# Performance work log

Hardware: AMD Instinct MI355X
Metric: run time of the kernel (lower is better)

## Reference

```python
import jax, jax.numpy as jnp
import numpy as np

N = 200000       # nodes
E = 6400000      # edges
F_IN, H1, H2, C = 7, 32, 16, 2


def gcn_conv(x, W, b, src, dst, n):
    """PyG GCNConv: add self-loops, symmetric normalization, linear, scatter-add."""
    loop = jnp.arange(n, dtype=src.dtype)
    s = jnp.concatenate([src, loop])
    d = jnp.concatenate([dst, loop])
    # degree of target nodes (with self-loops)
    deg = jax.ops.segment_sum(jnp.ones_like(d, dtype=x.dtype), d, num_segments=n)
    dinv = jnp.where(deg > 0, jax.lax.rsqrt(deg), 0.0)
    h = x @ W                                  # [n, out]
    norm = dinv[s] * dinv[d]                   # [e+n]
    msg = h[s] * norm[:, None]                 # gather + normalize
    out = jax.ops.segment_sum(msg, d, num_segments=n)  # scatter-add aggregation
    return out + b


def setup_inputs() -> dict:
    key = jax.random.key(0)
    ks = jax.random.split(key, 8)
    x = jax.random.normal(ks[0], (N, F_IN), dtype=jnp.float32)
    edge_index = jax.random.randint(ks[1], (2, E), 0, N, dtype=jnp.int64)
    def glorot(k, fan_in, fan_out):
        lim = np.sqrt(6.0 / (fan_in + fan_out)).astype(np.float32)
        return jax.random.uniform(k, (fan_in, fan_out), jnp.float32, -lim, lim)
    return {
        "x": x,
        "edge_index": edge_index,
        "W1": glorot(ks[2], F_IN, H1), "b1": jnp.zeros((H1,), jnp.float32),
        "W2": glorot(ks[3], H1, H2), "b2": jnp.zeros((H2,), jnp.float32),
        "Wfc": glorot(ks[4], H2, C), "bfc": jnp.zeros((C,), jnp.float32),
    }


def reference(x, edge_index, W1, b1, W2, b2, Wfc, bfc):
    src, dst = edge_index[0], edge_index[1]
    h = jax.nn.relu(gcn_conv(x, W1, b1, src, dst, N))
    h = jax.nn.relu(gcn_conv(h, W2, b2, src, dst, N))
    return h @ Wfc + bfc
```

## Files before the change

kernel.cpp:

```cpp
#include <hip/hip_runtime.h>

#define NNODES 200000
#define NEDGES 6400000
#define FIN 7
#define FH1 32
#define FH2 16
#define NC 2

#define WB 128
#define WB_SHIFT 7
#define NBUCK ((NNODES + WB - 1) / WB)
#define NBLK 512
#define CHUNK ((NEDGES + NBLK - 1) / NBLK)
#define PSHIFT 18
#define SRCMASK ((1u << PSHIFT) - 1)

#define SCAP 5120

#define SCAN_N (NBUCK * NBLK)
#define SCAN_ITEMS 16
#define SCAN_TILE (256 * SCAN_ITEMS)
#define SCAN_NT ((SCAN_N + SCAN_TILE - 1) / SCAN_TILE)


__global__ __launch_bounds__(256) void p1_count(const int* __restrict__ ei,
                                                int* __restrict__ counts) {
    __shared__ int h[NBUCK];
    for (int i = threadIdx.x; i < NBUCK; i += 256) h[i] = 0;
    __syncthreads();
    int base = blockIdx.x * CHUNK;
    int end = base + CHUNK;
    if (end > NEDGES) end = NEDGES;
    for (int e = base + threadIdx.x; e < end; e += 256) {
        int d = ei[NEDGES + e];
        atomicAdd(&h[d >> WB_SHIFT], 1);
    }
    __syncthreads();
    for (int i = threadIdx.x; i < NBUCK; i += 256)
        counts[i * NBLK + blockIdx.x] = h[i];
}


__global__ __launch_bounds__(256) void scan_sums(const int* __restrict__ in,
                                                 int* __restrict__ part) {
    int base = blockIdx.x * SCAN_TILE + threadIdx.x * SCAN_ITEMS;
    int s = 0;
#pragma unroll
    for (int k = 0; k < SCAN_ITEMS; ++k) {
        int idx = base + k;
        if (idx < SCAN_N) s += in[idx];
    }
    __shared__ int sm[256];
    sm[threadIdx.x] = s;
    __syncthreads();
    for (int off = 128; off > 0; off >>= 1) {
        if (threadIdx.x < off) sm[threadIdx.x] += sm[threadIdx.x + off];
        __syncthreads();
    }
    if (threadIdx.x == 0) part[blockIdx.x] = sm[0];
}

__global__ void scan_top_g(int* __restrict__ part) {
    if (threadIdx.x == 0 && blockIdx.x == 0) {
        int acc = 0;
        for (int i = 0; i < SCAN_NT; ++i) {
            int v = part[i];
            part[i] = acc;
            acc += v;
        }
    }
}

__global__ __launch_bounds__(256) void scan_write_g(const int* __restrict__ in,
                                                    const int* __restrict__ part,
                                                    int* __restrict__ out) {
    int t = threadIdx.x;
    int base = blockIdx.x * SCAN_TILE + t * SCAN_ITEMS;
    int local[SCAN_ITEMS];
    int s = 0;
#pragma unroll
    for (int k = 0; k < SCAN_ITEMS; ++k) {
        int idx = base + k;
        int v = (idx < SCAN_N) ? in[idx] : 0;
        local[k] = v;
        s += v;
    }
    __shared__ int sm[256];
    sm[t] = s;
    __syncthreads();
    for (int off = 1; off < 256; off <<= 1) {
        int v = (t >= off) ? sm[t - off] : 0;
        __syncthreads();
        sm[t] += v;
        __syncthreads();
    }
    int prefix = part[blockIdx.x] + sm[t] - s;
#pragma unroll
    for (int k = 0; k < SCAN_ITEMS; ++k) {
        int idx = base + k;
        if (idx < SCAN_N) {
            out[idx] = prefix;
            prefix += local[k];
        }
    }
}


__global__ __launch_bounds__(256) void p2_scatter(const int* __restrict__ ei,
                                                  const int* __restrict__ offs,
                                                  unsigned int* __restrict__ recs) {
    __shared__ int cur[NBUCK];
    for (int i = threadIdx.x; i < NBUCK; i += 256)
        cur[i] = offs[i * NBLK + blockIdx.x];
    __syncthreads();
    int base = blockIdx.x * CHUNK;
    int end = base + CHUNK;
    if (end > NEDGES) end = NEDGES;
    for (int e = base + threadIdx.x; e < end; e += 256) {
        int s = ei[e];
        int d = ei[NEDGES + e];
        int b = d >> WB_SHIFT;
        int slot = atomicAdd(&cur[b], 1);
        recs[slot] = (unsigned)s | ((unsigned)(d & (WB - 1)) << PSHIFT);
    }
}


__global__ __launch_bounds__(256) void p3_dinv(const unsigned int* __restrict__ recs,
                                               const int* __restrict__ offs,
                                               float* __restrict__ dinv) {
    __shared__ int h[WB];
    int b = blockIdx.x;
    if (threadIdx.x < WB) h[threadIdx.x] = 0;
    __syncthreads();
    int beg = offs[b * NBLK];
    int end = (b + 1 < NBUCK) ? offs[(b + 1) * NBLK] : NEDGES;
    for (int e = beg + threadIdx.x; e < end; e += 256)
        atomicAdd(&h[recs[e] >> PSHIFT], 1);
    __syncthreads();
    int node = b * WB + threadIdx.x;
    if (threadIdx.x < WB && node < NNODES)
        dinv[node] = rsqrtf((float)(1 + h[threadIdx.x]));
}


__global__ __launch_bounds__(256) void gx_kernel(const float* __restrict__ x,
                                                 const float* __restrict__ dinv,
                                                 float4* __restrict__ gx) {
    int i = blockIdx.x * blockDim.x + threadIdx.x;
    if (i >= NNODES) return;
    float di = dinv[i];
    const float* xr = x + (size_t)i * FIN;
    float4 v0, v1;
    v0.x = xr[0] * di; v0.y = xr[1] * di; v0.z = xr[2] * di; v0.w = xr[3] * di;
    v1.x = xr[4] * di; v1.y = xr[5] * di; v1.z = xr[6] * di; v1.w = 0.0f;
    gx[(size_t)i * 2 + 0] = v0;
    gx[(size_t)i * 2 + 1] = v1;
}


__global__ __launch_bounds__(256) void l1_sorted(const unsigned int* __restrict__ recs,
                                                 const int* __restrict__ offs,
                                                 const float4* __restrict__ gx,
                                                 const float* __restrict__ dinv,
                                                 const float* __restrict__ W1,
                                                 const float* __restrict__ b1,
                                                 const float* __restrict__ W2,
                                                 float4* __restrict__ y) {
    __shared__ int sl_src[SCAP];
    __shared__ int hist[WB], st[WB], cur[WB];
    __shared__ float acc[WB][9];
    __shared__ float sW1[FIN * FH1];
    __shared__ float sb1[FH1];
    __shared__ float sW2[FH1 * FH2];
    int t = threadIdx.x;
    for (int i = t; i < FIN * FH1; i += 256) sW1[i] = W1[i];
    if (t < FH1) sb1[t] = b1[t];
    for (int i = t; i < FH1 * FH2; i += 256) sW2[i] = W2[i];
    if (t < WB) hist[t] = 0;
    __syncthreads();

    int b = blockIdx.x;
    int beg = offs[b * NBLK];
    int end = (b + 1 < NBUCK) ? offs[(b + 1) * NBLK] : NEDGES;

    for (int e = beg + t; e < end; e += 256)
        atomicAdd(&hist[recs[e] >> PSHIFT], 1);
    __syncthreads();

    if (t < WB) cur[t] = hist[t];
    __syncthreads();
    for (int off = 1; off < WB; off <<= 1) {
        int v = 0;
        if (t < WB && t >= off) v = cur[t - off];
        __syncthreads();
        if (t < WB) cur[t] += v;
        __syncthreads();
    }
    if (t < WB) {
        st[t] = cur[t] - hist[t];
        cur[t] = cur[t] - hist[t];
    }
    __syncthreads();

    for (int e = beg + t; e < end; e += 256) {
        unsigned r = recs[e];
        int slot = atomicAdd(&cur[r >> PSHIFT], 1);
        sl_src[slot] = (int)(r & SRCMASK);
    }
    __syncthreads();

    int n = t >> 1;
    int hq = t & 1;
    int cnt = hist[n];
    int base = st[n];
    float ax = 0.0f, ay = 0.0f, az = 0.0f, aw = 0.0f;
    int k = 0;
    for (; k + 3 < cnt; k += 4) {
        int s0 = sl_src[base + k];
        int s1 = sl_src[base + k + 1];
        int s2 = sl_src[base + k + 2];
        int s3 = sl_src[base + k + 3];
        float4 v0 = gx[(size_t)s0 * 2 + hq];
        float4 v1 = gx[(size_t)s1 * 2 + hq];
        float4 v2 = gx[(size_t)s2 * 2 + hq];
        float4 v3 = gx[(size_t)s3 * 2 + hq];
        ax += v0.x + v1.x; ay += v0.y + v1.y;
        az += v0.z + v1.z; aw += v0.w + v1.w;
        ax += v2.x + v3.x; ay += v2.y + v3.y;
        az += v2.z + v3.z; aw += v2.w + v3.w;
    }
    for (; k < cnt; ++k) {
        int s0 = sl_src[base + k];
        float4 v0 = gx[(size_t)s0 * 2 + hq];
        ax += v0.x; ay += v0.y; az += v0.z; aw += v0.w;
    }
    int kb = hq * 4;
    acc[n][kb + 0] = ax; acc[n][kb + 1] = ay;
    acc[n][kb + 2] = az; acc[n][kb + 3] = aw;
    __syncthreads();

    int node = b * WB + t;
    if (t >= WB || node >= NNODES) return;

    float di = dinv[node];
    float4 g0 = gx[(size_t)node * 2], g1 = gx[(size_t)node * 2 + 1];
    float xa[FIN];
    xa[0] = (acc[t][0] + g0.x) * di;
    xa[1] = (acc[t][1] + g0.y) * di;
    xa[2] = (acc[t][2] + g0.z) * di;
    xa[3] = (acc[t][3] + g0.w) * di;
    xa[4] = (acc[t][4] + g1.x) * di;
    xa[5] = (acc[t][5] + g1.y) * di;
    xa[6] = (acc[t][6] + g1.z) * di;

    float h1[FH1];
#pragma unroll
    for (int j = 0; j < FH1; ++j) h1[j] = sb1[j];
#pragma unroll
    for (int f = 0; f < FIN; ++f) {
        float xv = xa[f];
#pragma unroll
        for (int j = 0; j < FH1; ++j) h1[j] = fmaf(xv, sW1[f * FH1 + j], h1[j]);
    }
#pragma unroll
    for (int j = 0; j < FH1; ++j) h1[j] = fmaxf(h1[j], 0.0f);

    float yv[FH2];
#pragma unroll
    for (int j = 0; j < FH2; ++j) yv[j] = 0.0f;
#pragma unroll
    for (int k2 = 0; k2 < FH1; ++k2) {
        float hv = h1[k2];
#pragma unroll
        for (int j = 0; j < FH2; ++j) yv[j] = fmaf(hv, sW2[k2 * FH2 + j], yv[j]);
    }

    size_t yb = (size_t)node * 4;
    float4 o;
    o.x = yv[0] * di; o.y = yv[1] * di; o.z = yv[2] * di; o.w = yv[3] * di;
    y[yb + 0] = o;
    o.x = yv[4] * di; o.y = yv[5] * di; o.z = yv[6] * di; o.w = yv[7] * di;
    y[yb + 1] = o;
    o.x = yv[8] * di; o.y = yv[9] * di; o.z = yv[10] * di; o.w = yv[11] * di;
    y[yb + 2] = o;
    o.x = yv[12] * di; o.y = yv[13] * di; o.z = yv[14] * di; o.w = yv[15] * di;
    y[yb + 3] = o;
}


__global__ __launch_bounds__(256) void l2_sorted(const unsigned int* __restrict__ recs,
                                                 const int* __restrict__ offs,
                                                 const float4* __restrict__ y,
                                                 const float* __restrict__ dinv,
                                                 const float* __restrict__ b2,
                                                 const float* __restrict__ Wfc,
                                                 const float* __restrict__ bfc,
                                                 float2* __restrict__ out) {
    __shared__ int sl_src[SCAP];
    __shared__ int hist[WB], st[WB], cur[WB];
    __shared__ float acc[WB][17];
    __shared__ float sb2[FH2];
    __shared__ float sWfc[FH2 * NC];
    __shared__ float sbfc[NC];
    int t = threadIdx.x;
    if (t < FH2) sb2[t] = b2[t];
    if (t < FH2 * NC) sWfc[t] = Wfc[t];
    if (t < NC) sbfc[t] = bfc[t];
    if (t < WB) hist[t] = 0;
    __syncthreads();

    int b = blockIdx.x;
    int beg = offs[b * NBLK];
    int end = (b + 1 < NBUCK) ? offs[(b + 1) * NBLK] : NEDGES;

    for (int e = beg + t; e < end; e += 256)
        atomicAdd(&hist[recs[e] >> PSHIFT], 1);
    __syncthreads();

    if (t < WB) cur[t] = hist[t];
    __syncthreads();
    for (int off = 1; off < WB; off <<= 1) {
        int v = 0;
        if (t < WB && t >= off) v = cur[t - off];
        __syncthreads();
        if (t < WB) cur[t] += v;
        __syncthreads();
    }
    if (t < WB) {
        st[t] = cur[t] - hist[t];
        cur[t] = cur[t] - hist[t];
    }
    __syncthreads();

    for (int e = beg + t; e < end; e += 256) {
        unsigned r = recs[e];
        int slot = atomicAdd(&cur[r >> PSHIFT], 1);
        sl_src[slot] = (int)(r & SRCMASK);
    }
    __syncthreads();

    int q = t & 3;
#pragma unroll
    for (int r = 0; r < 2; ++r) {
        int n = (t >> 2) + 64 * r;
        int cnt = hist[n];
        int base = st[n];
        float ax = 0.0f, ay = 0.0f, az = 0.0f, aw = 0.0f;
        int k = 0;
        for (; k + 3 < cnt; k += 4) {
            int s0 = sl_src[base + k];
            int s1 = sl_src[base + k + 1];
            int s2 = sl_src[base + k + 2];
            int s3 = sl_src[base + k + 3];
            float4 v0 = y[(size_t)s0 * 4 + q];
            float4 v1 = y[(size_t)s1 * 4 + q];
            float4 v2 = y[(size_t)s2 * 4 + q];
            float4 v3 = y[(size_t)s3 * 4 + q];
            ax += v0.x + v1.x; ay += v0.y + v1.y;
            az += v0.z + v1.z; aw += v0.w + v1.w;
            ax += v2.x + v3.x; ay += v2.y + v3.y;
            az += v2.z + v3.z; aw += v2.w + v3.w;
        }
        for (; k < cnt; ++k) {
            int s0 = sl_src[base + k];
            float4 v0 = y[(size_t)s0 * 4 + q];
            ax += v0.x; ay += v0.y; az += v0.z; aw += v0.w;
        }
        int kb = q * 4;
        acc[n][kb + 0] = ax; acc[n][kb + 1] = ay;
        acc[n][kb + 2] = az; acc[n][kb + 3] = aw;
    }
    __syncthreads();

    int node = b * WB + t;
    if (t >= WB || node >= NNODES) return;

    float di = dinv[node];
    size_t yb = (size_t)node * 4;
    float4 s0 = y[yb + 0], s1 = y[yb + 1], s2 = y[yb + 2], s3 = y[yb + 3];
    float self[FH2] = {s0.x, s0.y, s0.z, s0.w, s1.x, s1.y, s1.z, s1.w,
                       s2.x, s2.y, s2.z, s2.w, s3.x, s3.y, s3.z, s3.w};

    float o0 = sbfc[0], o1 = sbfc[1];
#pragma unroll
    for (int k = 0; k < FH2; ++k) {
        float h = fmaxf(fmaf(di, acc[t][k] + self[k], sb2[k]), 0.0f);
        o0 = fmaf(h, sWfc[k * NC + 0], o0);
        o1 = fmaf(h, sWfc[k * NC + 1], o1);
    }
    float2 ov; ov.x = o0; ov.y = o1;
    out[node] = ov;
}


extern "C" void kernel_launch(void* const* d_in, const int* in_sizes, int n_in,
                              void* d_out, int out_size, void* d_ws, size_t ws_size,
                              hipStream_t stream) {
    const float* x   = (const float*)d_in[0];
    const int*   ei  = (const int*)d_in[1];
    const float* W1  = (const float*)d_in[2];
    const float* b1  = (const float*)d_in[3];
    const float* W2  = (const float*)d_in[4];
    const float* b2  = (const float*)d_in[5];
    const float* Wfc = (const float*)d_in[6];
    const float* bfc = (const float*)d_in[7];
    float* out = (float*)d_out;

    char* p = (char*)d_ws;
    auto carve = [&](size_t bytes) -> char* {
        char* r = p;
        p += (bytes + 255) & ~(size_t)255;
        return r;
    };
    int*      counts = (int*)carve((size_t)SCAN_N * 4);
    int*      part   = (int*)carve(256 * 4);
    float*    dinv   = (float*)carve((size_t)NNODES * 4);
    float*    gx     = (float*)carve((size_t)NNODES * 8 * 4);
    float*    y      = (float*)carve((size_t)NNODES * 16 * 4);
    unsigned* recs   = (unsigned*)carve((size_t)NEDGES * 4);
    int* offs = counts;

    int nblocks = (NNODES + 255) / 256;

    p1_count<<<NBLK, 256, 0, stream>>>(ei, counts);
    scan_sums<<<SCAN_NT, 256, 0, stream>>>(counts, part);
    scan_top_g<<<1, 64, 0, stream>>>(part);
    scan_write_g<<<SCAN_NT, 256, 0, stream>>>(counts, part, offs);
    p2_scatter<<<NBLK, 256, 0, stream>>>(ei, offs, recs);
    p3_dinv<<<NBUCK, 256, 0, stream>>>(recs, offs, dinv);
    gx_kernel<<<nblocks, 256, 0, stream>>>(x, dinv, (float4*)gx);
    l1_sorted<<<NBUCK, 256, 0, stream>>>(recs, offs, (const float4*)gx, dinv,
                                         W1, b1, W2, (float4*)y);
    l2_sorted<<<NBUCK, 256, 0, stream>>>(recs, offs, (const float4*)y, dinv,
                                         b2, Wfc, bfc, (float2*)out);
}
```

Baseline: 412.2 us.

## Stage per-block bucket sort in LDS before writing coalesced records

The scatter kernel now computes each block's per-bucket counts from the global offsets, runs a block-local exclusive scan over them, and sorts its chunk of edges into shared memory first. It then writes the records out in bucket order, using a binary search to find each slot's bucket, so that global stores land in contiguous runs instead of scattered single-word writes. The cost is much more LDS (a CHUNK-sized buffer plus three arrays), extra syncs and scan work, a binary search per element, and possibly lower occupancy.

After: 382.1 us. -7.3%, faster.

```diff
diff --git a/kernel.cpp b/kernel.cpp
--- a/kernel.cpp
+++ b/kernel.cpp
@@ -109,19 +109,68 @@
 __global__ __launch_bounds__(256) void p2_scatter(const int* __restrict__ ei,
                                                   const int* __restrict__ offs,
                                                   unsigned int* __restrict__ recs) {
-    __shared__ int cur[NBUCK];
-    for (int i = threadIdx.x; i < NBUCK; i += 256)
-        cur[i] = offs[i * NBLK + blockIdx.x];
-    __syncthreads();
-    int base = blockIdx.x * CHUNK;
-    int end = base + CHUNK;
-    if (end > NEDGES) end = NEDGES;
-    for (int e = base + threadIdx.x; e < end; e += 256) {
-        int s = ei[e];
+    __shared__ int sorted[CHUNK];
+    __shared__ int lcur[NBUCK];
+    __shared__ int gbase[NBUCK];
+    __shared__ int sm[256];
+    int t = threadIdx.x;
+    int blk = blockIdx.x;
+
+    for (int b = t; b < NBUCK; b += 256) {
+        int g = offs[b * NBLK + blk];
+        gbase[b] = g;
+        int nxt;
+        if (blk + 1 < NBLK) nxt = offs[b * NBLK + blk + 1];
+        else nxt = (b + 1 < NBUCK) ? offs[(b + 1) * NBLK] : NEDGES;
+        lcur[b] = nxt - g;
+    }
+    __syncthreads();
+
+    int base7 = t * 7;
+    int loc[7];
+    int s = 0;
+#pragma unroll
+    for (int k = 0; k < 7; ++k) {
+        int idx = base7 + k;
+        int v = (idx < NBUCK) ? lcur[idx] : 0;
+        loc[k] = v;
+        s += v;
+    }
+    sm[t] = s;
+    __syncthreads();
+    for (int off = 1; off < 256; off <<= 1) {
+        int v = (t >= off) ? sm[t - off] : 0;
+        __syncthreads();
+        sm[t] += v;
+        __syncthreads();
+    }
+    int run = sm[t] - s;
+#pragma unroll
+    for (int k = 0; k < 7; ++k) {
+        int idx = base7 + k;
+        if (idx < NBUCK) { lcur[idx] = run; run += loc[k]; }
+    }
+    __syncthreads();
+
+    int ebase = blk * CHUNK;
+    for (int e = ebase + t; e < ebase + CHUNK; e += 256) {
+        int src = ei[e];
         int d = ei[NEDGES + e];
         int b = d >> WB_SHIFT;
-        int slot = atomicAdd(&cur[b], 1);
-        recs[slot] = (unsigned)s | ((unsigned)(d & (WB - 1)) << PSHIFT);
+        int slot = atomicAdd(&lcur[b], 1);
+        sorted[slot] = (int)((unsigned)src | ((unsigned)(d & (WB - 1)) << PSHIFT));
+    }
+    __syncthreads();
+
+    for (int i = t; i < CHUNK; i += 256) {
+        int lo = 0, hi = NBUCK - 1;
+        while (lo < hi) {
+            int mid = (lo + hi) >> 1;
+            if (lcur[mid] > i) hi = mid; else lo = mid + 1;
+        }
+        int b = lo;
+        int start = (b > 0) ? lcur[b - 1] : 0;
+        recs[gbase[b] + (i - start)] = (unsigned)sorted[i];
     }
 }
 
```
